# Optimization experiments

Measured on AMD Instinct MI355X. Metric: run time of the kernel, lower is better.

Reference implementation:

```python
import jax, jax.numpy as jnp
import numpy as np

N = 40000      # nodes
E = 640000     # edges
G = 2048       # graphs
D = 128        # emb_dim
T = 10         # num_tasks
L = 5          # layers
ATOM_VOCAB = 64
BOND_VOCAB = 8
BN_EPS = 1e-5


def _bn(x, g, b, m, v):
    # inference-mode BatchNorm1d with running stats
    return (x - m) * jax.lax.rsqrt(v + BN_EPS) * g + b


def setup_inputs() -> dict:
    key = jax.random.key(0)
    ks = jax.random.split(key, 24)
    inp = {
        "x_atom": jax.random.randint(ks[0], (N, 9), 0, ATOM_VOCAB),
        "edge_index": jax.random.randint(ks[1], (2, E), 0, N),
        "edge_attr": jax.random.randint(ks[2], (E, 3), 0, BOND_VOCAB),
        "batch": jnp.sort(jax.random.randint(ks[3], (N,), 0, G)),
        # embedding tables
        "atom_emb": jax.random.normal(ks[4], (9, ATOM_VOCAB, D)) * 0.1,
        "bond_emb": jax.random.normal(ks[5], (L, 3, BOND_VOCAB, D)) * 0.1,
        # per-layer GIN params (stacked over L)
        "eps": jnp.zeros((L,)),
        "W1": jax.random.normal(ks[6], (L, D, 2 * D)) * 0.05,
        "b1": jnp.zeros((L, 2 * D)),
        "g1": jnp.ones((L, 2 * D)),
        "bt1": jnp.zeros((L, 2 * D)),
        "m1": jax.random.normal(ks[7], (L, 2 * D)) * 0.1,
        "v1": jax.random.uniform(ks[8], (L, 2 * D), minval=0.5, maxval=1.5),
        "W2": jax.random.normal(ks[9], (L, 2 * D, D)) * 0.05,
        "b2": jnp.zeros((L, D)),
        # outer BatchNorm per layer
        "gO": jnp.ones((L, D)),
        "btO": jnp.zeros((L, D)),
        "mO": jax.random.normal(ks[10], (L, D)) * 0.1,
        "vO": jax.random.uniform(ks[11], (L, D), minval=0.5, maxval=1.5),
        # prediction head
        "Wp": jax.random.normal(ks[12], (D, T)) * 0.05,
        "bp": jnp.zeros((T,)),
    }
    return inp


def reference(x_atom, edge_index, edge_attr, batch, atom_emb, bond_emb, eps,
              W1, b1, g1, bt1, m1, v1, W2, b2, gO, btO, mO, vO, Wp, bp):
    src, dst = edge_index[0], edge_index[1]
    # AtomEncoder: sum of per-feature embeddings -> [N, D]
    x = atom_emb[jnp.arange(9)[None, :], x_atom].sum(axis=1)
    feat3 = jnp.arange(3)[None, :]
    for i in range(L):
        # BondEncoder for this layer -> [E, D]
        e = bond_emb[i][feat3, edge_attr].sum(axis=1)
        # message: relu(x_j + edge_emb); aggregate: scatter-add at dst
        msg = jax.nn.relu(x[src] + e)
        agg = jax.ops.segment_sum(msg, dst, num_segments=N)
        h = (1.0 + eps[i]) * x + agg
        # MLP: Linear -> BN -> ReLU -> Linear
        h = jax.nn.relu(_bn(h @ W1[i] + b1[i], g1[i], bt1[i], m1[i], v1[i]))
        h = h @ W2[i] + b2[i]
        # outer BN; ReLU after all but last layer (dropout = identity in eval)
        x = _bn(h, gO[i], btO[i], mO[i], vO[i])
        if i < L - 1:
            x = jax.nn.relu(x)
    # global mean pool over graphs
    sums = jax.ops.segment_sum(x, batch, num_segments=G)
    cnt = jax.ops.segment_sum(jnp.ones((N,), x.dtype), batch, num_segments=G)
    pooled = sums / jnp.maximum(cnt, 1.0)[:, None]
    return pooled @ Wp + bp
```

## Files before the change

### kernel.cpp

```cpp
#include <hip/hip_runtime.h>
#include <hip/hip_bf16.h>

#define NN 40000
#define NE 640000
#define NG 2048
#define DD 128
#define NT 10
#define NL 5
#define NB 80

typedef __attribute__((ext_vector_type(8))) short short8;
typedef __attribute__((ext_vector_type(8))) float f32x8;
typedef __attribute__((ext_vector_type(4))) float f32x4;
typedef unsigned short ushort_t;
typedef unsigned char uchar_t;

static __device__ __forceinline__ ushort_t f2b(float f) {
    return __bfloat16_as_ushort(__float2bfloat16(f));
}
static __device__ __forceinline__ float b2f(ushort_t u) {
    return __bfloat162float(__ushort_as_bfloat16(u));
}
static __device__ __forceinline__ uchar_t f2p8(float f) {
    return (uchar_t)(__builtin_amdgcn_cvt_pk_fp8_f32(f, 0.f, 0, false) & 0xFF);
}

__global__ void __launch_bounds__(256)
k_setup(const float* __restrict__ W1, const float* __restrict__ W2,
        const float* __restrict__ bemb, const int* __restrict__ xa,
        const float* __restrict__ aemb, const int* __restrict__ ei,
        ushort_t* __restrict__ W1P, ushort_t* __restrict__ W2P,
        ushort_t* __restrict__ ebsum16, ushort_t* __restrict__ x16,
        uchar_t* __restrict__ x8, int* __restrict__ gcnt) {
    int b = blockIdx.x, t = threadIdx.x;
    if (b < 1280) {
        int tid = b * 256 + t;
        int layer = tid >> 16;
        int r = tid & 65535;
        int half = r >> 15;
        int q = r & 32767;
        int j = q & 7;
        int lane = (q >> 3) & 63;
        if (half == 0) {
            int kk = (q >> 9) & 3;
            int nt = q >> 11;
            int n = nt * 16 + (lane & 15);
            int k = kk * 32 + (lane >> 4) * 8 + j;
            W1P[layer * 32768 + q] = f2b(W1[(layer * DD + k) * 256 + n]);
        } else {
            int kk = (q >> 9) & 7;
            int nt = q >> 12;
            int n = nt * 16 + (lane & 15);
            int k = kk * 32 + (lane >> 4) * 8 + j;
            W2P[layer * 32768 + q] = f2b(W2[(layer * 256 + k) * DD + n]);
        }
        int d = tid & 127;
        int c = (tid >> 7) & 511;
        const float* bl = bemb + (size_t)layer * 3 * 8 * DD;
        ebsum16[tid] = f2b(bl[(c & 7) * DD + d] + bl[(8 + ((c >> 3) & 7)) * DD + d] +
                           bl[(16 + (c >> 6)) * DD + d]);
    } else if (b < 3780) {
        int bb = b - 1280;
        __shared__ int idxS[144];
        if (t < 144) idxS[t] = xa[bb * 144 + t];
        __syncthreads();
        int nl = t >> 4, dcol = t & 15;
        int n = bb * 16 + nl;
        float acc[8];
#pragma unroll
        for (int k = 0; k < 8; ++k) acc[k] = 0.f;
#pragma unroll
        for (int f = 0; f < 9; ++f) {
            const f32x8 v = *(const f32x8*)&aemb[(f * 64 + idxS[nl * 9 + f]) * DD + dcol * 8];
#pragma unroll
            for (int k = 0; k < 8; ++k) acc[k] += v[k];
        }
        short8 o16;
#pragma unroll
        for (int k = 0; k < 8; ++k) o16[k] = (short)f2b(acc[k]);
        *(short8*)&x16[(size_t)n * DD + dcol * 8] = o16;
        unsigned int lo = 0, hi = 0;
        lo = __builtin_amdgcn_cvt_pk_fp8_f32(acc[0], acc[1], lo, false);
        lo = __builtin_amdgcn_cvt_pk_fp8_f32(acc[2], acc[3], lo, true);
        hi = __builtin_amdgcn_cvt_pk_fp8_f32(acc[4], acc[5], hi, false);
        hi = __builtin_amdgcn_cvt_pk_fp8_f32(acc[6], acc[7], hi, true);
        *(uint2*)&x8[(size_t)n * DD + dcol * 8] = make_uint2(lo, hi);
    } else {
        __shared__ int hist[NB];
        int e0 = (b - 3780) * 1024;
        if (t < NB) hist[t] = 0;
        __syncthreads();
#pragma unroll
        for (int k = 0; k < 4; ++k) {
            int e = e0 + k * 256 + t;
            atomicAdd(&hist[ei[NE + e] >> 9], 1);
        }
        __syncthreads();
        if (t < NB) atomicAdd(&gcnt[t], hist[t]);
    }
}

__global__ void k_bscan(const int* __restrict__ gcnt, int* __restrict__ bbase) {
    int t = threadIdx.x;
    __shared__ int s[128];
    int v = (t < NB) ? gcnt[t] : 0;
    s[t] = v;
    __syncthreads();
    for (int d = 1; d < 128; d <<= 1) {
        int add = (t >= d) ? s[t - d] : 0;
        __syncthreads();
        s[t] += add;
        __syncthreads();
    }
    if (t <= NB) bbase[t] = s[t] - v;
}

__global__ void __launch_bounds__(256)
k_bucket(const int* __restrict__ ei, const int* __restrict__ ea,
         const int* __restrict__ bbase, int* __restrict__ gbk,
         int2* __restrict__ ebuf) {
    __shared__ int hist[NB];
    __shared__ int sbase[NB];
    int t = threadIdx.x;
    int e0 = blockIdx.x * 1024;
    if (t < NB) hist[t] = 0;
    __syncthreads();
    int rank[4], buck[4], rec[4], dstv[4];
#pragma unroll
    for (int k = 0; k < 4; ++k) {
        int e = e0 + k * 256 + t;
        int src = ei[e];
        int dst = ei[NE + e];
        int a0 = ea[e * 3 + 0], a1 = ea[e * 3 + 1], a2 = ea[e * 3 + 2];
        rec[k] = src | ((a0 | (a1 << 3) | (a2 << 6)) << 16);
        dstv[k] = dst;
        int b = dst >> 9;
        buck[k] = b;
        rank[k] = atomicAdd(&hist[b], 1);
    }
    __syncthreads();
    if (t < NB) sbase[t] = atomicAdd(&gbk[t], hist[t]);
    __syncthreads();
#pragma unroll
    for (int k = 0; k < 4; ++k) {
        int b = buck[k];
        int slot = bbase[b] + sbase[b] + rank[k];
        ebuf[slot] = make_int2(rec[k], dstv[k]);
    }
}

__global__ void __launch_bounds__(256)
k_csr(const int2* __restrict__ ebuf, const int* __restrict__ bbase,
      int* __restrict__ off, int* __restrict__ epack) {
    __shared__ int cnt[512];
    __shared__ int cur[512];
    __shared__ int sc[256];
    int b = blockIdx.x, t = threadIdx.x;
    int base = bbase[b], end = bbase[b + 1];
    cnt[t] = 0; cnt[t + 256] = 0;
    cur[t] = 0; cur[t + 256] = 0;
    __syncthreads();
    for (int i = base + t; i < end; i += 256)
        atomicAdd(&cnt[ebuf[i].y & 511], 1);
    __syncthreads();
    int a = cnt[2 * t], c2 = cnt[2 * t + 1];
    sc[t] = a + c2;
    __syncthreads();
    for (int d = 1; d < 256; d <<= 1) {
        int add = (t >= d) ? sc[t - d] : 0;
        __syncthreads();
        sc[t] += add;
        __syncthreads();
    }
    int ex = sc[t] - (a + c2);
    cnt[2 * t] = ex;
    cnt[2 * t + 1] = ex + a;
    int n0 = (b << 9) + 2 * t;
    if (n0 <= NN) off[n0] = base + ex;
    if (n0 + 1 <= NN) off[n0 + 1] = base + ex + a;
    __syncthreads();
    for (int i = base + t; i < end; i += 256) {
        int2 s = ebuf[i];
        int l = s.y & 511;
        int r = atomicAdd(&cur[l], 1);
        epack[base + cnt[l] + r] = s.x;
    }
}

__global__ void __launch_bounds__(256)
k_gather(const ushort_t* __restrict__ xin, const uchar_t* __restrict__ x8in,
         const int* __restrict__ off, const int* __restrict__ epack,
         const ushort_t* __restrict__ ebsum16, const float* __restrict__ eps,
         int layer, ushort_t* __restrict__ h16) {
    int t = threadIdx.x;
    int lane = t & 63;
    int n = blockIdx.x * 4 + (t >> 6);
    const ushort2* x2 = (const ushort2*)xin;
    const ushort_t* x8r = (const ushort_t*)x8in;
    const ushort2* eb2 = (const ushort2*)ebsum16;
    ushort2 xv = x2[n * 64 + lane];
    float es = 1.f + eps[layer];
    float ax = es * b2f(xv.x), ay = es * b2f(xv.y);
    int p = off[n], p1 = off[n + 1];

    int e[8], f[8];
    bool have = (p + 8 <= p1);
    if (have) {
#pragma unroll
        for (int k = 0; k < 8; ++k) e[k] = epack[p + k];
    }
    while (have) {
        int np = p + 8;
        bool nh = (np + 8 <= p1);
        if (nh) {
#pragma unroll
            for (int k = 0; k < 8; ++k) f[k] = epack[np + k];
        }
        ushort2 vv[8];
        ushort_t sp[8];
#pragma unroll
        for (int k = 0; k < 8; ++k) {
            vv[k] = eb2[(e[k] >> 16) * 64 + lane];
            sp[k] = x8r[(e[k] & 0xFFFF) * 64 + lane];
        }
#pragma unroll
        for (int k = 0; k < 8; ++k) {
            float sx = __builtin_amdgcn_cvt_f32_fp8((int)sp[k], 0);
            float sy = __builtin_amdgcn_cvt_f32_fp8((int)sp[k], 1);
            ax += fmaxf(b2f(vv[k].x) + sx, 0.f);
            ay += fmaxf(b2f(vv[k].y) + sy, 0.f);
        }
        p = np;
#pragma unroll
        for (int k = 0; k < 8; ++k) e[k] = f[k];
        have = nh;
    }
    if (p + 4 <= p1) {
        int e4[4];
#pragma unroll
        for (int k = 0; k < 4; ++k) e4[k] = epack[p + k];
        ushort2 vv[4];
        ushort_t sp[4];
#pragma unroll
        for (int k = 0; k < 4; ++k) {
            vv[k] = eb2[(e4[k] >> 16) * 64 + lane];
            sp[k] = x8r[(e4[k] & 0xFFFF) * 64 + lane];
        }
#pragma unroll
        for (int k = 0; k < 4; ++k) {
            float sx = __builtin_amdgcn_cvt_f32_fp8((int)sp[k], 0);
            float sy = __builtin_amdgcn_cvt_f32_fp8((int)sp[k], 1);
            ax += fmaxf(b2f(vv[k].x) + sx, 0.f);
            ay += fmaxf(b2f(vv[k].y) + sy, 0.f);
        }
        p += 4;
    }
    for (; p < p1; ++p) {
        int er = epack[p];
        ushort2 ev = eb2[(er >> 16) * 64 + lane];
        ushort_t sv = x8r[(er & 0xFFFF) * 64 + lane];
        ax += fmaxf(b2f(ev.x) + __builtin_amdgcn_cvt_f32_fp8((int)sv, 0), 0.f);
        ay += fmaxf(b2f(ev.y) + __builtin_amdgcn_cvt_f32_fp8((int)sv, 1), 0.f);
    }
    ushort2 o;
    o.x = f2b(ax);
    o.y = f2b(ay);
    ((ushort2*)h16)[n * 64 + lane] = o;
}

__global__ void __launch_bounds__(256)
k_mlp_mfma(const ushort_t* __restrict__ h16, const ushort_t* __restrict__ W1P,
           const ushort_t* __restrict__ W2P, const float* __restrict__ b1,
           const float* __restrict__ g1, const float* __restrict__ bt1,
           const float* __restrict__ m1, const float* __restrict__ v1,
           const float* __restrict__ b2_, const float* __restrict__ gO,
           const float* __restrict__ btO, const float* __restrict__ mO,
           const float* __restrict__ vO, int relu, ushort_t* __restrict__ xout,
           uchar_t* __restrict__ x8out) {
    __shared__ ushort_t aS[32 * 136];
    __shared__ ushort_t mid[32 * 264];
    int t = threadIdx.x;
    int wave = t >> 6, lane = t & 63;
    int row0 = blockIdx.x * 32;
    int lrow = lane & 15, quad = lane >> 4;

#pragma unroll
    for (int ps = 0; ps < 2; ++ps) {
        int idx = ps * 256 + t;
        int r = idx >> 4, c = (idx & 15) * 8;
        *(short8*)&aS[r * 136 + c] = *(const short8*)&h16[(row0 + r) * DD + c];
    }
    __syncthreads();

    f32x4 acc1[2][4];
#pragma unroll
    for (int rt = 0; rt < 2; ++rt)
#pragma unroll
        for (int i = 0; i < 4; ++i) acc1[rt][i] = (f32x4){0.f, 0.f, 0.f, 0.f};
#pragma unroll
    for (int kk = 0; kk < 4; ++kk) {
        short8 af0 = *(const short8*)&aS[lrow * 136 + kk * 32 + quad * 8];
        short8 af1 = *(const short8*)&aS[(16 + lrow) * 136 + kk * 32 + quad * 8];
#pragma unroll
        for (int i = 0; i < 4; ++i) {
            int nt = wave * 4 + i;
            short8 bf = *(const short8*)&W1P[((nt * 4 + kk) * 64 + lane) * 8];
            acc1[0][i] = __builtin_amdgcn_mfma_f32_16x16x32_bf16(af0, bf, acc1[0][i], 0, 0, 0);
            acc1[1][i] = __builtin_amdgcn_mfma_f32_16x16x32_bf16(af1, bf, acc1[1][i], 0, 0, 0);
        }
    }
    __syncthreads();
#pragma unroll
    for (int i = 0; i < 4; ++i) {
        int col = (wave * 4 + i) * 16 + lrow;
        float s1 = g1[col] * rsqrtf(v1[col] + 1e-5f);
        float sh = bt1[col] - (m1[col] - b1[col]) * s1;
#pragma unroll
        for (int rt = 0; rt < 2; ++rt)
#pragma unroll
            for (int r = 0; r < 4; ++r) {
                int row = rt * 16 + quad * 4 + r;
                float o = acc1[rt][i][r] * s1 + sh;
                mid[row * 264 + col] = f2b(fmaxf(o, 0.f));
            }
    }
    __syncthreads();

    f32x4 acc2[2][2];
#pragma unroll
    for (int rt = 0; rt < 2; ++rt)
#pragma unroll
        for (int i = 0; i < 2; ++i) acc2[rt][i] = (f32x4){0.f, 0.f, 0.f, 0.f};
#pragma unroll
    for (int kk = 0; kk < 8; ++kk) {
        short8 af0 = *(const short8*)&mid[lrow * 264 + kk * 32 + quad * 8];
        short8 af1 = *(const short8*)&mid[(16 + lrow) * 264 + kk * 32 + quad * 8];
#pragma unroll
        for (int i = 0; i < 2; ++i) {
            int nt = wave * 2 + i;
            short8 bf = *(const short8*)&W2P[((nt * 8 + kk) * 64 + lane) * 8];
            acc2[0][i] = __builtin_amdgcn_mfma_f32_16x16x32_bf16(af0, bf, acc2[0][i], 0, 0, 0);
            acc2[1][i] = __builtin_amdgcn_mfma_f32_16x16x32_bf16(af1, bf, acc2[1][i], 0, 0, 0);
        }
    }
    uchar_t* s8 = (uchar_t*)aS;
#pragma unroll
    for (int i = 0; i < 2; ++i) {
        int col = (wave * 2 + i) * 16 + lrow;
        float s = gO[col] * rsqrtf(vO[col] + 1e-5f);
        float sh = btO[col] - (mO[col] - b2_[col]) * s;
#pragma unroll
        for (int rt = 0; rt < 2; ++rt)
#pragma unroll
            for (int r = 0; r < 4; ++r) {
                int row = rt * 16 + quad * 4 + r;
                float o = acc2[rt][i][r] * s + sh;
                if (relu) o = fmaxf(o, 0.f);
                xout[(row0 + row) * DD + col] = f2b(o);
                s8[row * DD + col] = f2p8(o);
            }
    }
    __syncthreads();
    ((int4*)(x8out + (size_t)row0 * DD))[t] = ((const int4*)s8)[t];
}

__global__ void k_poolhead(const ushort_t* __restrict__ x16,
                           const int* __restrict__ batch,
                           const float* __restrict__ Wp, const float* __restrict__ bp,
                           float* __restrict__ out) {
    int g = blockIdx.x, d = threadIdx.x;
    int lo = 0, hi = NN;
    while (lo < hi) { int m = (lo + hi) >> 1; if (batch[m] < g) lo = m + 1; else hi = m; }
    int start = lo;
    hi = NN;
    while (lo < hi) { int m = (lo + hi) >> 1; if (batch[m] < g + 1) lo = m + 1; else hi = m; }
    int end = lo;
    float s = 0.f;
    for (int n = start; n < end; ++n) s += b2f(x16[n * DD + d]);
    float c = fmaxf((float)(end - start), 1.f);
    __shared__ float p[DD];
    p[d] = s / c;
    __syncthreads();
    if (d < NT) {
        float acc = bp[d];
#pragma unroll 8
        for (int k = 0; k < DD; ++k) acc = fmaf(p[k], Wp[k * NT + d], acc);
        out[g * NT + d] = acc;
    }
}

extern "C" void kernel_launch(void* const* d_in, const int* in_sizes, int n_in,
                              void* d_out, int out_size, void* d_ws, size_t ws_size,
                              hipStream_t stream) {
    const int* x_atom = (const int*)d_in[0];
    const int* edge_index = (const int*)d_in[1];
    const int* edge_attr = (const int*)d_in[2];
    const int* batch = (const int*)d_in[3];
    const float* atom_emb = (const float*)d_in[4];
    const float* bond_emb = (const float*)d_in[5];
    const float* eps = (const float*)d_in[6];
    const float* W1 = (const float*)d_in[7];
    const float* b1 = (const float*)d_in[8];
    const float* g1 = (const float*)d_in[9];
    const float* bt1 = (const float*)d_in[10];
    const float* m1 = (const float*)d_in[11];
    const float* v1 = (const float*)d_in[12];
    const float* W2 = (const float*)d_in[13];
    const float* b2 = (const float*)d_in[14];
    const float* gO = (const float*)d_in[15];
    const float* btO = (const float*)d_in[16];
    const float* mO = (const float*)d_in[17];
    const float* vO = (const float*)d_in[18];
    const float* Wp = (const float*)d_in[19];
    const float* bp = (const float*)d_in[20];

    ushort_t* x16a = (ushort_t*)d_ws;
    ushort_t* x16b = x16a + NN * DD;
    ushort_t* h16 = x16b + NN * DD;
    ushort_t* W1P = h16 + NN * DD;
    ushort_t* W2P = W1P + NL * 32768;
    ushort_t* ebsum16 = W2P + NL * 32768;
    uchar_t* x8a = (uchar_t*)(ebsum16 + NL * 65536);
    uchar_t* x8b = x8a + NN * DD;
    int* off = (int*)(x8b + NN * DD);
    int* gcnt = off + 40064;
    int* gbk = gcnt + 80;
    int* bbase = gbk + 80;
    int* epack = bbase + 128;
    int2* ebuf = (int2*)(epack + NE);

    hipMemsetAsync(gcnt, 0, 160 * sizeof(int), stream);

    k_setup<<<4405, 256, 0, stream>>>(W1, W2, bond_emb, x_atom, atom_emb,
                                      edge_index, W1P, W2P, ebsum16, x16a, x8a, gcnt);
    k_bscan<<<1, 128, 0, stream>>>(gcnt, bbase);
    k_bucket<<<NE / 1024, 256, 0, stream>>>(edge_index, edge_attr, bbase, gbk, ebuf);
    k_csr<<<NB, 256, 0, stream>>>(ebuf, bbase, off, epack);

    for (int i = 0; i < NL; ++i) {
        ushort_t* xin = (i & 1) ? x16b : x16a;
        ushort_t* xout = (i & 1) ? x16a : x16b;
        uchar_t* x8in = (i & 1) ? x8b : x8a;
        uchar_t* x8out = (i & 1) ? x8a : x8b;
        k_gather<<<NN / 4, 256, 0, stream>>>(xin, x8in, off, epack,
                                             ebsum16 + i * 65536, eps, i, h16);
        k_mlp_mfma<<<NN / 32, 256, 0, stream>>>(
            h16, W1P + (size_t)i * 32768, W2P + (size_t)i * 32768, b1 + i * 256,
            g1 + i * 256, bt1 + i * 256, m1 + i * 256, v1 + i * 256, b2 + i * DD,
            gO + i * DD, btO + i * DD, mO + i * DD, vO + i * DD,
            (i < NL - 1) ? 1 : 0, xout, x8out);
    }
    k_poolhead<<<NG, DD, 0, stream>>>(x16b, batch, Wp, bp, (float*)d_out);
}
```

Before: 383.2 us.

## Fuse bucket scan into consumers, split gather edges across half-waves, widen pool

Removes the single-block bucket-scan kernel by recomputing the 80-entry prefix sum inside the bucket and CSR kernels, saving one launch. The gather kernel now has each half-wave handle alternate edges with 4 features per lane (wider loads), then combines halves with a cross-lane shuffle, raising memory-level parallelism per node. The pool/head kernel uses 256 threads with four node-strided partial sums. Costs are redundant scan work in every block and a shuffle reduction per node.

```diff
diff --git a/kernel.cpp b/kernel.cpp
--- a/kernel.cpp
+++ b/kernel.cpp
@@ -100,31 +100,28 @@
     }
 }
 
-__global__ void k_bscan(const int* __restrict__ gcnt, int* __restrict__ bbase) {
-    int t = threadIdx.x;
-    __shared__ int s[128];
-    int v = (t < NB) ? gcnt[t] : 0;
-    s[t] = v;
-    __syncthreads();
-    for (int d = 1; d < 128; d <<= 1) {
-        int add = (t >= d) ? s[t - d] : 0;
-        __syncthreads();
-        s[t] += add;
-        __syncthreads();
-    }
-    if (t <= NB) bbase[t] = s[t] - v;
-}
-
 __global__ void __launch_bounds__(256)
 k_bucket(const int* __restrict__ ei, const int* __restrict__ ea,
-         const int* __restrict__ bbase, int* __restrict__ gbk,
+         const int* __restrict__ gcnt, int* __restrict__ gbk,
          int2* __restrict__ ebuf) {
     __shared__ int hist[NB];
     __shared__ int sbase[NB];
+    __shared__ int sB[128];
+    __shared__ int exS[NB];
     int t = threadIdx.x;
+    if (t < NB) hist[t] = 0;
+    int v0 = 0;
+    if (t < 128) { v0 = (t < NB) ? gcnt[t] : 0; sB[t] = v0; }
+    __syncthreads();
+    for (int d = 1; d < 128; d <<= 1) {
+        int add = (t < 128 && t >= d) ? sB[t - d] : 0;
+        __syncthreads();
+        if (t < 128) sB[t] += add;
+        __syncthreads();
+    }
+    if (t < NB) exS[t] = sB[t] - v0;
+    __syncthreads();
     int e0 = blockIdx.x * 1024;
-    if (t < NB) hist[t] = 0;
-    __syncthreads();
     int rank[4], buck[4], rec[4], dstv[4];
 #pragma unroll
     for (int k = 0; k < 4; ++k) {
@@ -144,21 +141,32 @@
 #pragma unroll
     for (int k = 0; k < 4; ++k) {
         int b = buck[k];
-        int slot = bbase[b] + sbase[b] + rank[k];
+        int slot = exS[b] + sbase[b] + rank[k];
         ebuf[slot] = make_int2(rec[k], dstv[k]);
     }
 }
 
 __global__ void __launch_bounds__(256)
-k_csr(const int2* __restrict__ ebuf, const int* __restrict__ bbase,
+k_csr(const int2* __restrict__ ebuf, const int* __restrict__ gcnt,
       int* __restrict__ off, int* __restrict__ epack) {
     __shared__ int cnt[512];
     __shared__ int cur[512];
     __shared__ int sc[256];
+    __shared__ int sB[128];
     int b = blockIdx.x, t = threadIdx.x;
-    int base = bbase[b], end = bbase[b + 1];
+    int v0 = 0;
+    if (t < 128) { v0 = (t < NB) ? gcnt[t] : 0; sB[t] = v0; }
     cnt[t] = 0; cnt[t + 256] = 0;
     cur[t] = 0; cur[t + 256] = 0;
+    __syncthreads();
+    for (int d = 1; d < 128; d <<= 1) {
+        int add = (t < 128 && t >= d) ? sB[t - d] : 0;
+        __syncthreads();
+        if (t < 128) sB[t] += add;
+        __syncthreads();
+    }
+    int base = sB[b] - gcnt[b];
+    int end = base + gcnt[b];
     __syncthreads();
     for (int i = base + t; i < end; i += 256)
         atomicAdd(&cnt[ebuf[i].y & 511], 1);
@@ -194,78 +202,96 @@
          int layer, ushort_t* __restrict__ h16) {
     int t = threadIdx.x;
     int lane = t & 63;
+    int half = lane >> 5;
+    int q = lane & 31;
     int n = blockIdx.x * 4 + (t >> 6);
-    const ushort2* x2 = (const ushort2*)xin;
-    const ushort_t* x8r = (const ushort_t*)x8in;
-    const ushort2* eb2 = (const ushort2*)ebsum16;
-    ushort2 xv = x2[n * 64 + lane];
-    float es = 1.f + eps[layer];
-    float ax = es * b2f(xv.x), ay = es * b2f(xv.y);
+    const ushort4* eb4 = (const ushort4*)ebsum16;
+    const uint* xu = (const uint*)x8in;
+    const ushort4* x4 = (const ushort4*)xin;
+    ushort4 xv = x4[(size_t)n * 32 + q];
+    float acc[4];
+#pragma unroll
+    for (int k = 0; k < 4; ++k) acc[k] = 0.f;
     int p = off[n], p1 = off[n + 1];
 
-    int e[8], f[8];
-    bool have = (p + 8 <= p1);
+    int rec[8], recn[8];
+    bool have = (p + 16 <= p1);
     if (have) {
 #pragma unroll
-        for (int k = 0; k < 8; ++k) e[k] = epack[p + k];
+        for (int j = 0; j < 8; ++j) rec[j] = epack[p + 2 * j + half];
     }
     while (have) {
-        int np = p + 8;
-        bool nh = (np + 8 <= p1);
+        int np = p + 16;
+        bool nh = (np + 16 <= p1);
         if (nh) {
 #pragma unroll
-            for (int k = 0; k < 8; ++k) f[k] = epack[np + k];
-        }
-        ushort2 vv[8];
-        ushort_t sp[8];
-#pragma unroll
-        for (int k = 0; k < 8; ++k) {
-            vv[k] = eb2[(e[k] >> 16) * 64 + lane];
-            sp[k] = x8r[(e[k] & 0xFFFF) * 64 + lane];
-        }
-#pragma unroll
-        for (int k = 0; k < 8; ++k) {
-            float sx = __builtin_amdgcn_cvt_f32_fp8((int)sp[k], 0);
-            float sy = __builtin_amdgcn_cvt_f32_fp8((int)sp[k], 1);
-            ax += fmaxf(b2f(vv[k].x) + sx, 0.f);
-            ay += fmaxf(b2f(vv[k].y) + sy, 0.f);
+            for (int j = 0; j < 8; ++j) recn[j] = epack[np + 2 * j + half];
+        }
+        ushort4 vv[8];
+        uint ss[8];
+#pragma unroll
+        for (int j = 0; j < 8; ++j) {
+            vv[j] = eb4[(rec[j] >> 16) * 32 + q];
+            ss[j] = xu[(size_t)(rec[j] & 0xFFFF) * 32 + q];
+        }
+#pragma unroll
+        for (int j = 0; j < 8; ++j) {
+            acc[0] += fmaxf(b2f(vv[j].x) + __builtin_amdgcn_cvt_f32_fp8((int)ss[j], 0), 0.f);
+            acc[1] += fmaxf(b2f(vv[j].y) + __builtin_amdgcn_cvt_f32_fp8((int)ss[j], 1), 0.f);
+            acc[2] += fmaxf(b2f(vv[j].z) + __builtin_amdgcn_cvt_f32_fp8((int)ss[j], 2), 0.f);
+            acc[3] += fmaxf(b2f(vv[j].w) + __builtin_amdgcn_cvt_f32_fp8((int)ss[j], 3), 0.f);
         }
         p = np;
 #pragma unroll
-        for (int k = 0; k < 8; ++k) e[k] = f[k];
+        for (int j = 0; j < 8; ++j) rec[j] = recn[j];
         have = nh;
     }
-    if (p + 4 <= p1) {
-        int e4[4];
-#pragma unroll
-        for (int k = 0; k < 4; ++k) e4[k] = epack[p + k];
-        ushort2 vv[4];
-        ushort_t sp[4];
-#pragma unroll
-        for (int k = 0; k < 4; ++k) {
-            vv[k] = eb2[(e4[k] >> 16) * 64 + lane];
-            sp[k] = x8r[(e4[k] & 0xFFFF) * 64 + lane];
-        }
-#pragma unroll
-        for (int k = 0; k < 4; ++k) {
-            float sx = __builtin_amdgcn_cvt_f32_fp8((int)sp[k], 0);
-            float sy = __builtin_amdgcn_cvt_f32_fp8((int)sp[k], 1);
-            ax += fmaxf(b2f(vv[k].x) + sx, 0.f);
-            ay += fmaxf(b2f(vv[k].y) + sy, 0.f);
-        }
-        p += 4;
-    }
-    for (; p < p1; ++p) {
-        int er = epack[p];
-        ushort2 ev = eb2[(er >> 16) * 64 + lane];
-        ushort_t sv = x8r[(er & 0xFFFF) * 64 + lane];
-        ax += fmaxf(b2f(ev.x) + __builtin_amdgcn_cvt_f32_fp8((int)sv, 0), 0.f);
-        ay += fmaxf(b2f(ev.y) + __builtin_amdgcn_cvt_f32_fp8((int)sv, 1), 0.f);
-    }
-    ushort2 o;
-    o.x = f2b(ax);
-    o.y = f2b(ay);
-    ((ushort2*)h16)[n * 64 + lane] = o;
+    if (p + 8 <= p1) {
+        int r4[4];
+#pragma unroll
+        for (int j = 0; j < 4; ++j) r4[j] = epack[p + 2 * j + half];
+        ushort4 vv[4];
+        uint ss[4];
+#pragma unroll
+        for (int j = 0; j < 4; ++j) {
+            vv[j] = eb4[(r4[j] >> 16) * 32 + q];
+            ss[j] = xu[(size_t)(r4[j] & 0xFFFF) * 32 + q];
+        }
+#pragma unroll
+        for (int j = 0; j < 4; ++j) {
+            acc[0] += fmaxf(b2f(vv[j].x) + __builtin_amdgcn_cvt_f32_fp8((int)ss[j], 0), 0.f);
+            acc[1] += fmaxf(b2f(vv[j].y) + __builtin_amdgcn_cvt_f32_fp8((int)ss[j], 1), 0.f);
+            acc[2] += fmaxf(b2f(vv[j].z) + __builtin_amdgcn_cvt_f32_fp8((int)ss[j], 2), 0.f);
+            acc[3] += fmaxf(b2f(vv[j].w) + __builtin_amdgcn_cvt_f32_fp8((int)ss[j], 3), 0.f);
+        }
+        p += 8;
+    }
+    for (; p < p1; p += 2) {
+        int eA = epack[p];
+        bool hasB = (p + 1 < p1);
+        int eB = hasB ? epack[p + 1] : eA;
+        int r = half ? eB : eA;
+        bool valid = half ? hasB : true;
+        ushort4 v = eb4[(r >> 16) * 32 + q];
+        uint s = xu[(size_t)(r & 0xFFFF) * 32 + q];
+        if (valid) {
+            acc[0] += fmaxf(b2f(v.x) + __builtin_amdgcn_cvt_f32_fp8((int)s, 0), 0.f);
+            acc[1] += fmaxf(b2f(v.y) + __builtin_amdgcn_cvt_f32_fp8((int)s, 1), 0.f);
+            acc[2] += fmaxf(b2f(v.z) + __builtin_amdgcn_cvt_f32_fp8((int)s, 2), 0.f);
+            acc[3] += fmaxf(b2f(v.w) + __builtin_amdgcn_cvt_f32_fp8((int)s, 3), 0.f);
+        }
+    }
+#pragma unroll
+    for (int k = 0; k < 4; ++k) acc[k] += __shfl_xor(acc[k], 32, 64);
+    if (half == 0) {
+        float es = 1.f + eps[layer];
+        ushort4 o;
+        o.x = f2b(acc[0] + es * b2f(xv.x));
+        o.y = f2b(acc[1] + es * b2f(xv.y));
+        o.z = f2b(acc[2] + es * b2f(xv.z));
+        o.w = f2b(acc[3] + es * b2f(xv.w));
+        ((ushort4*)h16)[(size_t)n * 32 + q] = o;
+    }
 }
 
 __global__ void __launch_bounds__(256)
@@ -368,24 +394,36 @@
                            const int* __restrict__ batch,
                            const float* __restrict__ Wp, const float* __restrict__ bp,
                            float* __restrict__ out) {
-    int g = blockIdx.x, d = threadIdx.x;
+    int g = blockIdx.x, t = threadIdx.x;
+    int j = t >> 6, l = t & 63;
     int lo = 0, hi = NN;
     while (lo < hi) { int m = (lo + hi) >> 1; if (batch[m] < g) lo = m + 1; else hi = m; }
     int start = lo;
     hi = NN;
     while (lo < hi) { int m = (lo + hi) >> 1; if (batch[m] < g + 1) lo = m + 1; else hi = m; }
     int end = lo;
-    float s = 0.f;
-    for (int n = start; n < end; ++n) s += b2f(x16[n * DD + d]);
-    float c = fmaxf((float)(end - start), 1.f);
-    __shared__ float p[DD];
-    p[d] = s / c;
-    __syncthreads();
-    if (d < NT) {
-        float acc = bp[d];
+    const ushort2* x2 = (const ushort2*)x16;
+    float sx = 0.f, sy = 0.f;
+    for (int n = start + j; n < end; n += 4) {
+        ushort2 v = x2[(size_t)n * 64 + l];
+        sx += b2f(v.x);
+        sy += b2f(v.y);
+    }
+    __shared__ float pp[4][DD];
+    pp[j][2 * l] = sx;
+    pp[j][2 * l + 1] = sy;
+    __syncthreads();
+    __shared__ float pfin[DD];
+    if (t < DD) {
+        float c = fmaxf((float)(end - start), 1.f);
+        pfin[t] = (pp[0][t] + pp[1][t] + pp[2][t] + pp[3][t]) / c;
+    }
+    __syncthreads();
+    if (t < NT) {
+        float acc = bp[t];
 #pragma unroll 8
-        for (int k = 0; k < DD; ++k) acc = fmaf(p[k], Wp[k * NT + d], acc);
-        out[g * NT + d] = acc;
+        for (int k = 0; k < DD; ++k) acc = fmaf(pfin[k], Wp[k * NT + t], acc);
+        out[g * NT + t] = acc;
     }
 }
 
@@ -425,17 +463,15 @@
     int* off = (int*)(x8b + NN * DD);
     int* gcnt = off + 40064;
     int* gbk = gcnt + 80;
-    int* bbase = gbk + 80;
-    int* epack = bbase + 128;
+    int* epack = gbk + 80;
     int2* ebuf = (int2*)(epack + NE);
 
     hipMemsetAsync(gcnt, 0, 160 * sizeof(int), stream);
 
     k_setup<<<4405, 256, 0, stream>>>(W1, W2, bond_emb, x_atom, atom_emb,
                                       edge_index, W1P, W2P, ebsum16, x16a, x8a, gcnt);
-    k_bscan<<<1, 128, 0, stream>>>(gcnt, bbase);
-    k_bucket<<<NE / 1024, 256, 0, stream>>>(edge_index, edge_attr, bbase, gbk, ebuf);
-    k_csr<<<NB, 256, 0, stream>>>(ebuf, bbase, off, epack);
+    k_bucket<<<NE / 1024, 256, 0, stream>>>(edge_index, edge_attr, gcnt, gbk, ebuf);
+    k_csr<<<NB, 256, 0, stream>>>(ebuf, gcnt, off, epack);
 
     for (int i = 0; i < NL; ++i) {
         ushort_t* xin = (i & 1) ? x16b : x16a;
@@ -450,5 +486,5 @@
             gO + i * DD, btO + i * DD, mO + i * DD, vO + i * DD,
             (i < NL - 1) ? 1 : 0, xout, x8out);
     }
-    k_poolhead<<<NG, DD, 0, stream>>>(x16b, batch, Wp, bp, (float*)d_out);
-}
+    k_poolhead<<<NG, 256, 0, stream>>>(x16b, batch, Wp, bp, (float*)d_out);
+}
```

After: 382.5 us (median of 2 runs). No clear change (-0.2%).
